# Kernel tuning notes

Measured on AMD Instinct MI355X. Metric: run time of the kernel, lower is better.

The kernel has to match this reference:

```python
import jax, jax.numpy as jnp
import numpy as np

B, N, DK, DV = 16, 4096, 64, 64


def setup_inputs() -> dict:
    key = jax.random.key(0)
    kq, kk, kv = jax.random.split(key, 3)
    q = jax.random.normal(kq, (B, N, DK), dtype=jnp.float32)
    k = jax.random.normal(kk, (B, N, DK), dtype=jnp.float32)
    v = jax.random.normal(kv, (B, N, DV), dtype=jnp.float32)
    # causal mask: positions j<=i are attendable (mask==True)
    mask = jnp.tril(jnp.ones((N, N), dtype=bool))[None, :, :]  # (1, N, N)
    return {"q": q, "k": k, "v": v, "mask": mask}


def reference(q, k, v, mask):
    # scores: (B, N, N)
    scale = 1.0 / jnp.sqrt(jnp.asarray(q.shape[-1], dtype=q.dtype))
    scores = jnp.einsum('bnd,bmd->bnm', q, k) * scale
    scores = jnp.where(mask, scores, jnp.asarray(-jnp.inf, dtype=scores.dtype))
    attn = jax.nn.softmax(scores, axis=-1)
    # dropout is identity in eval/reference mode
    return jnp.einsum('bnm,bmd->bnd', attn, v)
```

## Files before the change

kernel.cpp:

```cpp
#include <hip/hip_runtime.h>


#define N_SEQ 4096
#define DIM   64

typedef __bf16  bf16x8 __attribute__((ext_vector_type(8)));
typedef unsigned short u16x8 __attribute__((ext_vector_type(8)));
typedef float   f32x4  __attribute__((ext_vector_type(4)));
typedef float   f32x16 __attribute__((ext_vector_type(16)));

static __device__ __forceinline__ unsigned short f2bf(float f) {
    unsigned int u = __float_as_uint(f);
    u += 0x7FFFu + ((u >> 16) & 1u);
    return (unsigned short)(u >> 16);
}

static __device__ __forceinline__ unsigned int pk2bf(float a, float b) {
#if defined(__HIP_DEVICE_COMPILE__) && __has_builtin(__builtin_amdgcn_cvt_pk_bf16_f32)
    typedef __bf16 bf16x2_t __attribute__((ext_vector_type(2)));
    bf16x2_t r = __builtin_amdgcn_cvt_pk_bf16_f32(a, b);
    return __builtin_bit_cast(unsigned int, r);
#else
    return (unsigned int)f2bf(a) | ((unsigned int)f2bf(b) << 16);
#endif
}

static __device__ __forceinline__ float fexp2(float x) {
#if defined(__HIP_DEVICE_COMPILE__) && __has_builtin(__builtin_amdgcn_exp2f)
    return __builtin_amdgcn_exp2f(x);
#else
    return exp2f(x);
#endif
}

static __device__ __forceinline__ bf16x8 ld_frag(const void* p) {
    u16x8 u = *reinterpret_cast<const u16x8*>(p);
    return __builtin_bit_cast(bf16x8, u);
}

static __device__ __forceinline__ f32x16 mfma32(bf16x8 a, bf16x8 b, f32x16 c) {
#if defined(__HIP_DEVICE_COMPILE__)
#if __has_builtin(__builtin_amdgcn_mfma_f32_32x32x16_bf16)
    return __builtin_amdgcn_mfma_f32_32x32x16_bf16(a, b, c, 0, 0, 0);
#else
    f32x16 d;
    asm volatile("v_mfma_f32_32x32x16_bf16 %0, %1, %2, %3"
                 : "=v"(d) : "v"(a), "v"(b), "v"(c));
    return d;
#endif
#else
    (void)a; (void)b;
    return c;
#endif
}

static __device__ __forceinline__ void gl_lds16(const unsigned short* g, unsigned short* l) {
#if defined(__HIP_DEVICE_COMPILE__)
    __builtin_amdgcn_global_load_lds(
        (const __attribute__((address_space(1))) unsigned int*)(g),
        (__attribute__((address_space(3))) unsigned int*)(l), 16, 0, 0);
#else
    (void)g; (void)l;
#endif
}

__global__ __launch_bounds__(256)
void prep_kv(const float* __restrict__ K, const float* __restrict__ V,
             unsigned short* __restrict__ wsK, unsigned short* __restrict__ wsV) {
    const int b = blockIdx.y, t = blockIdx.x;
    if (blockIdx.z == 0) {
        const float* src = K + ((size_t)b * N_SEQ + t * 64) * DIM;
        unsigned short* dst = wsK + ((size_t)(b * 64 + t)) * 4096;
        #pragma unroll
        for (int ph = 0; ph < 2; ++ph) {
            const int gidx = threadIdx.x + ph * 256;
            const int r = gidx >> 3, g = gidx & 7;
            const float* p = src + r * DIM + g * 8;
            f32x4 f0 = *reinterpret_cast<const f32x4*>(p);
            f32x4 f1 = *reinterpret_cast<const f32x4*>(p + 4);
            uint4 w;
            w.x = pk2bf(f0[0], f0[1]); w.y = pk2bf(f0[2], f0[3]);
            w.z = pk2bf(f1[0], f1[1]); w.w = pk2bf(f1[2], f1[3]);
            const int rp = (r & 51) | ((r & 4) << 1) | ((r & 8) >> 1);
            *reinterpret_cast<uint4*>(&dst[(rp * 8 + (g ^ (rp & 7))) * 8]) = w;
        }
    } else {
        const int dv = threadIdx.x & 63;
        const int g0 = threadIdx.x >> 6;
        const float* src = V + ((size_t)b * N_SEQ + t * 64) * DIM + dv;
        unsigned short* dst = wsV + ((size_t)(b * 64 + t)) * 4096 + dv * 64;
        #pragma unroll
        for (int ph = 0; ph < 2; ++ph) {
            const int c = g0 * 2 + ph;
            float p[8];
            #pragma unroll
            for (int e = 0; e < 8; ++e)
                p[e] = src[(size_t)(c * 8 + e) * DIM];
            uint4 w;
            w.x = pk2bf(p[0], p[1]); w.y = pk2bf(p[2], p[3]);
            w.z = pk2bf(p[4], p[5]); w.w = pk2bf(p[6], p[7]);
            *reinterpret_cast<uint4*>(&dst[(c ^ (dv & 7)) * 8]) = w;
        }
    }
}

__global__ __launch_bounds__(512, 1)
void attn_fwd(const float* __restrict__ Q, const unsigned short* __restrict__ wsK,
              const unsigned short* __restrict__ wsV, float* __restrict__ O,
              float* __restrict__ wsO, float* __restrict__ wsL) {
    __shared__ unsigned short smem[32768];

    const int tid  = threadIdx.x;
    const int wave = tid >> 6;
    const int lane = tid & 63;
    const int l31  = lane & 31;
    const int h    = lane >> 5;
    const int l7   = lane & 7;
    const int wq   = wave & 3;
    const int wk   = wave >> 2;

    const int L    = (int)blockIdx.x;
    const int r    = L & 7;
    const int w    = L >> 3;
    const int role = w & 1;
    const int bsel = (w >> 1) & 1;
    const int j    = w >> 2;
    const int b    = r * 2 + bsel;
    const int Tq   = 31 - j;

    int it_tile[2], it_k0[2], it_k1[2], it_half[2], n_items;
    if (role == 0) {
        it_tile[0] = j;   it_k0[0] = 0;          it_k1[0] = 2 * j + 2;  it_half[0] = -1;
        it_tile[1] = Tq;  it_k0[1] = 0;          it_k1[1] = 31 - 2 * j; it_half[1] = 0;
        n_items = 2;
    } else {
        it_tile[0] = Tq;  it_k0[0] = 31 - 2 * j; it_k1[0] = 64 - 2 * j; it_half[0] = 1;
        n_items = 1;
    }

    int kaddr[4];
    #pragma unroll
    for (int s = 0; s < 4; ++s)
        kaddr[s] = (wk * 32 + l31) * 128 + (((s * 2 + h) ^ l7) * 16);
    int vbase[2];
    #pragma unroll
    for (int t = 0; t < 2; ++t)
        vbase[t] = l31 * 128 + (((wk * 4 + t * 2 + h) ^ l7) * 16);

    const int dma_off = wave * 512 + lane * 8;
    const u16x8 ones_u = {0x3F80, 0x3F80, 0x3F80, 0x3F80,
                          0x3F80, 0x3F80, 0x3F80, 0x3F80};
    const bf16x8 ones8 = __builtin_bit_cast(bf16x8, ones_u);
    const float QS = 0.125f * 1.44269504f;

    const unsigned short* kt_src = wsK + (size_t)b * 64 * 4096;
    const unsigned short* vt_src = wsV + (size_t)b * 64 * 4096;

    for (int it = 0; it < n_items; ++it) {
        const int tt    = it_tile[it];
        const int kt0   = it_k0[it];
        const int kt1   = it_k1[it];
        const int half  = it_half[it];
        const int i0    = tt * 128;
        const int tdiag = 2 * tt;

        __syncthreads();

        f32x16 o_acc[2] = {};
        f32x16 lones = {};

        if (kt0 < kt1) {
            u16x8 qb[4];
            const float* qptr = Q + ((size_t)b * N_SEQ + i0 + wq * 32 + l31) * DIM;
            #pragma unroll
            for (int s = 0; s < 4; ++s) {
                const float* p = qptr + s * 16 + h * 8;
                f32x4 f0 = *reinterpret_cast<const f32x4*>(p);
                f32x4 f1 = *reinterpret_cast<const f32x4*>(p + 4);
                #pragma unroll
                for (int jj = 0; jj < 4; ++jj) {
                    qb[s][jj]     = f2bf(f0[jj] * QS);
                    qb[s][4 + jj] = f2bf(f1[jj] * QS);
                }
            }

            auto dma = [&](int kt) {
                const int sl = (kt & 3) * 4096;
                gl_lds16(kt_src + (size_t)kt * 4096 + dma_off, &smem[sl + dma_off]);
                gl_lds16(vt_src + (size_t)kt * 4096 + dma_off, &smem[16384 + sl + dma_off]);
            };

            auto compute = [&](int kt, const unsigned short* kb, const unsigned short* vb) {
                f32x16 st = {};
                #pragma unroll
                for (int s = 0; s < 4; ++s) {
                    bf16x8 kf = ld_frag((const char*)kb + kaddr[s]);
                    st = mfma32(kf, __builtin_bit_cast(bf16x8, qb[s]), st);
                }
                float pex[16];
                if (kt >= tdiag) {
                    const int qth = (i0 + wq * 32 + l31) - (kt * 64 + wk * 32 + 8 * h);
                    #pragma unroll
                    for (int rr = 0; rr < 16; ++rr) {
                        const int K0 = (rr & 7) | ((rr & 8) << 1);
                        pex[rr] = fexp2((K0 > qth) ? -3.0e38f : st[rr]);
                    }
                } else {
                    #pragma unroll
                    for (int rr = 0; rr < 16; ++rr)
                        pex[rr] = fexp2(st[rr]);
                }
                unsigned int u[8];
                #pragma unroll
                for (int g = 0; g < 4; ++g) {
                    u[2 * g]     = pk2bf(pex[4 * g],     pex[4 * g + 1]);
                    u[2 * g + 1] = pk2bf(pex[4 * g + 2], pex[4 * g + 3]);
                }
                #pragma unroll
                for (int t = 0; t < 2; ++t) {
                    uint4 aw = make_uint4(u[4 * t], u[4 * t + 1], u[4 * t + 2], u[4 * t + 3]);
                    bf16x8 pa = __builtin_bit_cast(bf16x8, aw);
                    #pragma unroll
                    for (int dvt = 0; dvt < 2; ++dvt) {
                        bf16x8 bv = ld_frag((const char*)vb + vbase[t] + dvt * 4096);
                        o_acc[dvt] = mfma32(pa, bv, o_acc[dvt]);
                    }
                    lones = mfma32(pa, ones8, lones);
                }
            };

            dma(kt0);
            if (kt0 + 1 < kt1) dma(kt0 + 1);
            if (kt0 + 2 < kt1) dma(kt0 + 2);

            int kt = kt0;
            while (true) {
                __builtin_amdgcn_s_barrier();
                __builtin_amdgcn_sched_barrier(0);
                if (kt + 3 < kt1) dma(kt + 3);
                {
                    const int rem = kt1 - kt;
                    if (rem > 3)       asm volatile("s_waitcnt vmcnt(6)" ::: "memory");
                    else if (rem == 3) asm volatile("s_waitcnt vmcnt(4)" ::: "memory");
                    else if (rem == 2) asm volatile("s_waitcnt vmcnt(2)" ::: "memory");
                    else               asm volatile("s_waitcnt vmcnt(0)" ::: "memory");
                }
                __builtin_amdgcn_sched_barrier(0);
                __builtin_amdgcn_s_barrier();
                __builtin_amdgcn_sched_barrier(0);
                const int sl = (kt & 3) * 4096;
                compute(kt, &smem[sl], &smem[16384 + sl]);
                if (++kt == kt1) break;
            }
        }

        __syncthreads();
        float* red   = reinterpret_cast<float*>(&smem[0]);
        float* lredX = red + 8192;
        if (wk == 1) {
            #pragma unroll
            for (int rr = 0; rr < 16; ++rr) {
                const int qrow = (rr & 3) + 8 * (rr >> 2) + 4 * h;
                #pragma unroll
                for (int dvt = 0; dvt < 2; ++dvt)
                    red[wq * 2048 + qrow * 64 + dvt * 32 + l31] = o_acc[dvt][rr];
                if (l31 == 0) lredX[wq * 32 + qrow] = lones[rr];
            }
        }
        __syncthreads();
        if (wk == 0) {
            if (half < 0) {
                float* obase = O + ((size_t)b * N_SEQ + i0 + wq * 32) * DIM;
                #pragma unroll
                for (int rr = 0; rr < 16; ++rr) {
                    const int qrow = (rr & 3) + 8 * (rr >> 2) + 4 * h;
                    const float lt = lones[rr] + lredX[wq * 32 + qrow];
                    const float inv = 1.0f / lt;
                    #pragma unroll
                    for (int dvt = 0; dvt < 2; ++dvt) {
                        const float val = o_acc[dvt][rr]
                            + red[wq * 2048 + qrow * 64 + dvt * 32 + l31];
                        obase[qrow * DIM + dvt * 32 + l31] = val * inv;
                    }
                }
            } else {
                float* po = wsO + (((size_t)(b * 16 + (tt - 16)) * 2 + half) * 8192);
                float* pl = wsL + (((size_t)(b * 16 + (tt - 16)) * 2 + half) * 128);
                #pragma unroll
                for (int rr = 0; rr < 16; ++rr) {
                    const int qrow = (rr & 3) + 8 * (rr >> 2) + 4 * h;
                    const float lt = lones[rr] + lredX[wq * 32 + qrow];
                    #pragma unroll
                    for (int dvt = 0; dvt < 2; ++dvt)
                        po[(wq * 32 + qrow) * 64 + dvt * 32 + l31] = o_acc[dvt][rr]
                            + red[wq * 2048 + qrow * 64 + dvt * 32 + l31];
                    if (l31 == 0) pl[wq * 32 + qrow] = lt;
                }
            }
        }
    }
}

__global__ __launch_bounds__(256)
void norm_out(const float* __restrict__ wsO, const float* __restrict__ wsL,
              float* __restrict__ O) {
    const int t = 16 + blockIdx.x, b = blockIdx.y;
    const int row = threadIdx.x >> 1;
    const int c0  = (threadIdx.x & 1) * 32;
    const size_t base = (size_t)(b * 16 + (t - 16)) * 2;
    const float* p0 = wsO + base * 8192 + row * 64 + c0;
    const float* p1 = p0 + 8192;
    const float* l  = wsL + base * 128;
    const float inv = 1.0f / (l[row] + l[128 + row]);
    float* o = O + ((size_t)b * N_SEQ + t * 128 + row) * 64 + c0;
    #pragma unroll
    for (int i = 0; i < 32; i += 4) {
        f32x4 a = *reinterpret_cast<const f32x4*>(p0 + i);
        f32x4 c = *reinterpret_cast<const f32x4*>(p1 + i);
        f32x4 v = (a + c) * inv;
        *reinterpret_cast<f32x4*>(o + i) = v;
    }
}

extern "C" void kernel_launch(void* const* d_in, const int* in_sizes, int n_in,
                              void* d_out, int out_size, void* d_ws, size_t ws_size,
                              hipStream_t stream) {
    const float* q = (const float*)d_in[0];
    const float* k = (const float*)d_in[1];
    const float* v = (const float*)d_in[2];
    float* out = (float*)d_out;

    unsigned short* wsK = (unsigned short*)d_ws;
    unsigned short* wsV = wsK + (size_t)16 * 64 * 4096;
    float* wsO = (float*)(wsV + (size_t)16 * 64 * 4096);
    float* wsL = wsO + (size_t)16 * 16 * 2 * 8192;

    prep_kv<<<dim3(64, 16, 2), dim3(256), 0, stream>>>(k, v, wsK, wsV);
    attn_fwd<<<dim3(512), dim3(512), 0, stream>>>(q, wsK, wsV, out, wsO, wsL);
    norm_out<<<dim3(16, 16), dim3(256), 0, stream>>>(wsO, wsL, out);
}
```

Measured before the change: 209.5 us.

## Software-pipeline PV of previous tile with QK/softmax of current; sum row in VALU

Splits the per-tile compute into a QK+exp stage and a PV stage, issuing the previous tile's PV MFMAs alongside the current tile's QK and exponentials so matrix and vector work can overlap. The prefetch distance drops from three tiles to two so the V buffer of the prior tile stays resident. The row-sum that used a third MFMA against a ones vector is replaced by per-lane VALU additions reduced through shared memory in the epilogue. This cuts MFMA count but adds VALU adds, extra LDS traffic and live registers, and the shallower prefetch may expose more load latency.

```diff
diff --git a/kernel.cpp b/kernel.cpp
--- a/kernel.cpp
+++ b/kernel.cpp
@@ -148,9 +148,6 @@
         vbase[t] = l31 * 128 + (((wk * 4 + t * 2 + h) ^ l7) * 16);
 
     const int dma_off = wave * 512 + lane * 8;
-    const u16x8 ones_u = {0x3F80, 0x3F80, 0x3F80, 0x3F80,
-                          0x3F80, 0x3F80, 0x3F80, 0x3F80};
-    const bf16x8 ones8 = __builtin_bit_cast(bf16x8, ones_u);
     const float QS = 0.125f * 1.44269504f;
 
     const unsigned short* kt_src = wsK + (size_t)b * 64 * 4096;
@@ -167,7 +164,8 @@
         __syncthreads();
 
         f32x16 o_acc[2] = {};
-        f32x16 lones = {};
+        unsigned int u[8];
+        float l_lane = 0.0f;
 
         if (kt0 < kt1) {
             u16x8 qb[4];
@@ -190,7 +188,20 @@
                 gl_lds16(vt_src + (size_t)kt * 4096 + dma_off, &smem[16384 + sl + dma_off]);
             };
 
-            auto compute = [&](int kt, const unsigned short* kb, const unsigned short* vb) {
+            auto pv = [&](const unsigned short* vb) {
+                #pragma unroll
+                for (int t = 0; t < 2; ++t) {
+                    uint4 aw = make_uint4(u[4 * t], u[4 * t + 1], u[4 * t + 2], u[4 * t + 3]);
+                    bf16x8 pa = __builtin_bit_cast(bf16x8, aw);
+                    #pragma unroll
+                    for (int dvt = 0; dvt < 2; ++dvt) {
+                        bf16x8 bv = ld_frag((const char*)vb + vbase[t] + dvt * 4096);
+                        o_acc[dvt] = mfma32(pa, bv, o_acc[dvt]);
+                    }
+                }
+            };
+
+            auto qksm = [&](int kt, const unsigned short* kb) {
                 f32x16 st = {};
                 #pragma unroll
                 for (int s = 0; s < 4; ++s) {
@@ -210,53 +221,56 @@
                     for (int rr = 0; rr < 16; ++rr)
                         pex[rr] = fexp2(st[rr]);
                 }
-                unsigned int u[8];
                 #pragma unroll
                 for (int g = 0; g < 4; ++g) {
                     u[2 * g]     = pk2bf(pex[4 * g],     pex[4 * g + 1]);
                     u[2 * g + 1] = pk2bf(pex[4 * g + 2], pex[4 * g + 3]);
                 }
-                #pragma unroll
-                for (int t = 0; t < 2; ++t) {
-                    uint4 aw = make_uint4(u[4 * t], u[4 * t + 1], u[4 * t + 2], u[4 * t + 3]);
-                    bf16x8 pa = __builtin_bit_cast(bf16x8, aw);
-                    #pragma unroll
-                    for (int dvt = 0; dvt < 2; ++dvt) {
-                        bf16x8 bv = ld_frag((const char*)vb + vbase[t] + dvt * 4096);
-                        o_acc[dvt] = mfma32(pa, bv, o_acc[dvt]);
-                    }
-                    lones = mfma32(pa, ones8, lones);
-                }
+                float s0 = (pex[0] + pex[1]) + (pex[2] + pex[3]);
+                float s1 = (pex[4] + pex[5]) + (pex[6] + pex[7]);
+                float s2 = (pex[8] + pex[9]) + (pex[10] + pex[11]);
+                float s3 = (pex[12] + pex[13]) + (pex[14] + pex[15]);
+                l_lane += (s0 + s1) + (s2 + s3);
             };
 
+            const int last0 = (kt1 - 1 < kt0 + 2) ? kt1 - 1 : kt0 + 2;
             dma(kt0);
-            if (kt0 + 1 < kt1) dma(kt0 + 1);
-            if (kt0 + 2 < kt1) dma(kt0 + 2);
-
-            int kt = kt0;
-            while (true) {
+            if (last0 > kt0)     dma(kt0 + 1);
+            if (last0 > kt0 + 1) dma(kt0 + 2);
+            {
+                const int inf = last0 - kt0;
+                if (inf == 2)      asm volatile("s_waitcnt vmcnt(4)" ::: "memory");
+                else if (inf == 1) asm volatile("s_waitcnt vmcnt(2)" ::: "memory");
+                else               asm volatile("s_waitcnt vmcnt(0)" ::: "memory");
+            }
+            __builtin_amdgcn_sched_barrier(0);
+            __builtin_amdgcn_s_barrier();
+            __builtin_amdgcn_sched_barrier(0);
+            qksm(kt0, &smem[(kt0 & 3) * 4096]);
+
+            for (int kt = kt0 + 1; kt < kt1; ++kt) {
                 __builtin_amdgcn_s_barrier();
                 __builtin_amdgcn_sched_barrier(0);
-                if (kt + 3 < kt1) dma(kt + 3);
+                if (kt + 2 < kt1) dma(kt + 2);
                 {
-                    const int rem = kt1 - kt;
-                    if (rem > 3)       asm volatile("s_waitcnt vmcnt(6)" ::: "memory");
-                    else if (rem == 3) asm volatile("s_waitcnt vmcnt(4)" ::: "memory");
-                    else if (rem == 2) asm volatile("s_waitcnt vmcnt(2)" ::: "memory");
+                    const int last = (kt1 - 1 < kt + 2) ? kt1 - 1 : kt + 2;
+                    const int inf  = last - kt;
+                    if (inf == 2)      asm volatile("s_waitcnt vmcnt(4)" ::: "memory");
+                    else if (inf == 1) asm volatile("s_waitcnt vmcnt(2)" ::: "memory");
                     else               asm volatile("s_waitcnt vmcnt(0)" ::: "memory");
                 }
                 __builtin_amdgcn_sched_barrier(0);
                 __builtin_amdgcn_s_barrier();
                 __builtin_amdgcn_sched_barrier(0);
-                const int sl = (kt & 3) * 4096;
-                compute(kt, &smem[sl], &smem[16384 + sl]);
-                if (++kt == kt1) break;
-            }
+                pv(&smem[16384 + ((kt - 1) & 3) * 4096]);
+                qksm(kt, &smem[(kt & 3) * 4096]);
+            }
+            pv(&smem[16384 + ((kt1 - 1) & 3) * 4096]);
         }
 
         __syncthreads();
-        float* red   = reinterpret_cast<float*>(&smem[0]);
-        float* lredX = red + 8192;
+        float* red  = reinterpret_cast<float*>(&smem[0]);
+        float* lsum = red + 8192;
         if (wk == 1) {
             #pragma unroll
             for (int rr = 0; rr < 16; ++rr) {
@@ -264,9 +278,9 @@
                 #pragma unroll
                 for (int dvt = 0; dvt < 2; ++dvt)
                     red[wq * 2048 + qrow * 64 + dvt * 32 + l31] = o_acc[dvt][rr];
-                if (l31 == 0) lredX[wq * 32 + qrow] = lones[rr];
-            }
-        }
+            }
+        }
+        lsum[(wk * 2 + h) * 128 + wq * 32 + l31] = l_lane;
         __syncthreads();
         if (wk == 0) {
             if (half < 0) {
@@ -274,7 +288,9 @@
                 #pragma unroll
                 for (int rr = 0; rr < 16; ++rr) {
                     const int qrow = (rr & 3) + 8 * (rr >> 2) + 4 * h;
-                    const float lt = lones[rr] + lredX[wq * 32 + qrow];
+                    const int qi   = wq * 32 + qrow;
+                    const float lt = (lsum[qi] + lsum[128 + qi])
+                                   + (lsum[256 + qi] + lsum[384 + qi]);
                     const float inv = 1.0f / lt;
                     #pragma unroll
                     for (int dvt = 0; dvt < 2; ++dvt) {
@@ -289,12 +305,14 @@
                 #pragma unroll
                 for (int rr = 0; rr < 16; ++rr) {
                     const int qrow = (rr & 3) + 8 * (rr >> 2) + 4 * h;
-                    const float lt = lones[rr] + lredX[wq * 32 + qrow];
+                    const int qi   = wq * 32 + qrow;
+                    const float lt = (lsum[qi] + lsum[128 + qi])
+                                   + (lsum[256 + qi] + lsum[384 + qi]);
                     #pragma unroll
                     for (int dvt = 0; dvt < 2; ++dvt)
-                        po[(wq * 32 + qrow) * 64 + dvt * 32 + l31] = o_acc[dvt][rr]
+                        po[qi * 64 + dvt * 32 + l31] = o_acc[dvt][rr]
                             + red[wq * 2048 + qrow * 64 + dvt * 32 + l31];
-                    if (l31 == 0) pl[wq * 32 + qrow] = lt;
+                    if (l31 == 0) pl[qi] = lt;
                 }
             }
         }
```

After: 213.4 us. Within noise of the previous version (+1.9%).
